# Kernel tuning notes

Hardware: AMD Instinct MI355X
Metric: run time of the kernel (lower is better)

Reference implementation:

```python
import jax, jax.numpy as jnp
import numpy as np

SHIFTS = [1, 3, 5, 7]
C = 16  # in_channels // 4
# -1 neighbor offsets for tmp1..tmp8 (dy, dx) in units of the dilation
OFFSETS = [(-1, -1), (-1, 0), (-1, 1), (0, 1), (1, 1), (1, 0), (1, -1), (0, -1)]


def setup_inputs() -> dict:
    key = jax.random.key(0)
    ks = jax.random.split(key, 32)
    d = {}
    d['cen'] = jax.random.normal(ks[0], (8, 64, 256, 256), jnp.float32)
    d['mas'] = jax.random.normal(ks[1], (8, 1, 256, 256), jnp.float32)
    d['in_conv_w'] = jax.random.normal(ks[2], (16, 64), jnp.float32) * 0.1
    d['in_conv_b'] = jax.random.normal(ks[3], (16,), jnp.float32) * 0.1
    for i, s in enumerate(SHIFTS):
        d[f'dw_w{s}'] = jax.random.normal(ks[4 + 2 * i], (16, 1, s, s), jnp.float32) * 0.1
        d[f'dw_b{s}'] = jax.random.normal(ks[5 + 2 * i], (16,), jnp.float32) * 0.1
    d['l1_w'] = jax.random.normal(ks[12], (4, 16, 4), jnp.float32) * 0.1
    d['l1_b'] = jax.random.normal(ks[13], (4, 16), jnp.float32) * 0.1
    d['l2_w'] = jax.random.normal(ks[14], (4, 16, 8), jnp.float32) * 0.1
    d['l2_b'] = jax.random.normal(ks[15], (4, 16), jnp.float32) * 0.1
    d['base_w'] = jax.random.normal(ks[16], (16, 4), jnp.float32) * 0.1
    d['bn_scale'] = jnp.ones((16,), jnp.float32)
    d['bn_bias'] = jnp.zeros((16,), jnp.float32)
    d['final_w'] = jax.random.normal(ks[17], (1, 16), jnp.float32) * 0.1
    d['final_b'] = jax.random.normal(ks[18], (1,), jnp.float32) * 0.1
    return d


def _dw_conv(x, w, b, pad):
    # depthwise conv, groups == channels
    y = jax.lax.conv_general_dilated(
        x, w, window_strides=(1, 1), padding=[(pad, pad), (pad, pad)],
        dimension_numbers=('NCHW', 'OIHW', 'NCHW'), feature_group_count=x.shape[1])
    return y + b[None, :, None, None]


def _shifted(x, dy, dx, d):
    # zero-padded shift: out(y,x) = in(y+dy, x+dx)
    H, W = x.shape[2], x.shape[3]
    p = jnp.pad(x, ((0, 0), (0, 0), (d, d), (d, d)))
    return p[:, :, d + dy:d + dy + H, d + dx:d + dx + W]


def _circ_shift(x, dw_w, dw_b, w1, b1, w2, b2, shift):
    x = _dw_conv(x, dw_w, dw_b, shift // 2)
    # tmp_k = x - x shifted by the k-th neighbor offset (dilation = shift)
    T = [x - _shifted(x, dy * shift, dx * shift, shift) for dy, dx in OFFSETS]
    # paired sums: S[k] = tmp_{k+1} + tmp_{k+5} (S repeats with period 4)
    S = [T[k] + T[k + 4] for k in range(4)]
    outs = []
    for k in range(8):  # fixed small structural loop
        feats = jnp.stack([S[(k + 1) % 4], S[(k + 3) % 4], S[(k + 2) % 4],
                           2.0 * T[(k + 4) % 8]], axis=2)  # (B,C,4,H,W)
        # grouped 1x1 conv (groups=C, 4C->C) == per-channel contraction over feature axis
        o = jnp.einsum('bcfhw,cf->bchw', feats, w1) + b1[None, :, None, None]
        outs.append(o * T[k])
    O = jnp.sort(jnp.stack(outs, axis=2), axis=2)  # (B,C,8,H,W) sorted over branch axis
    return jnp.einsum('bcfhw,cf->bchw', O, w2) + b2[None, :, None, None]


def reference(cen, mas, in_conv_w, in_conv_b, dw_w1, dw_b1, dw_w3, dw_b3,
              dw_w5, dw_b5, dw_w7, dw_b7, l1_w, l1_b, l2_w, l2_b,
              base_w, bn_scale, bn_bias, final_w, final_b):
    # in_conv: 1x1, in_channels -> C
    x = jnp.einsum('bihw,oi->bohw', cen, in_conv_w) + in_conv_b[None, :, None, None]
    dws = [(dw_w1, dw_b1), (dw_w3, dw_b3), (dw_w5, dw_b5), (dw_w7, dw_b7)]
    branches = [
        _circ_shift(x, dws[i][0], dws[i][1], l1_w[i], l1_b[i], l2_w[i], l2_b[i], SHIFTS[i])
        for i in range(len(SHIFTS))
    ]
    A = jnp.sort(jnp.stack(branches, axis=2), axis=2)  # (B,C,4,H,W)
    # out_conv: grouped 1x1 BaseConv (conv no-bias + BN(affine) + SiLU), then 1x1 -> 1, sigmoid
    y = jnp.einsum('bcfhw,cf->bchw', A, base_w)
    y = jax.nn.silu(y * bn_scale[None, :, None, None] + bn_bias[None, :, None, None])
    y = jnp.einsum('bchw,oc->bohw', y, final_w) + final_b[None, :, None, None]
    return jax.nn.sigmoid(y)
```

## Files before the change

kernel.cpp:

```cpp
#include <hip/hip_runtime.h>
#include <hip/hip_fp16.h>
#include <math.h>

#define HW 65536

typedef float v2f __attribute__((ext_vector_type(2), aligned(4)));
typedef _Float16 h2 __attribute__((ext_vector_type(2)));

__global__ __launch_bounds__(256) void k_inconv(const float* __restrict__ cen,
                                                const float* __restrict__ w,
                                                const float* __restrict__ bias,
                                                float* __restrict__ x) {
    __shared__ float sw[1024];
    __shared__ float sb[16];
    int tid = threadIdx.x;
    for (int i = tid; i < 1024; i += 256) sw[i] = w[i];
    if (tid < 16) sb[tid] = bias[tid];
    __syncthreads();

    long t  = (long)blockIdx.x * 256 + tid;
    long p0 = t * 2;
    int  b  = (int)(p0 >> 16);
    int  hw = (int)(p0 & 65535);

    const float2* src = (const float2*)(cen + ((long)b * 64) * HW + hw);
    float2 acc[16];
#pragma unroll
    for (int o = 0; o < 16; o++) { float bv = sb[o]; acc[o] = make_float2(bv, bv); }

#pragma unroll 8
    for (int i = 0; i < 64; i++) {
        float2 v = src[(long)i * (HW / 2)];
#pragma unroll
        for (int o = 0; o < 16; o++) {
            float wv = sw[o * 64 + i];
            acc[o].x = fmaf(v.x, wv, acc[o].x);
            acc[o].y = fmaf(v.y, wv, acc[o].y);
        }
    }
    float2* dst = (float2*)(x + ((long)b * 16) * HW + hw);
#pragma unroll
    for (int o = 0; o < 16; o++) dst[(long)o * (HW / 2)] = acc[o];
}

#define CEH(a, b) { h2 _t = __builtin_elementwise_min(a, b); \
                    b = __builtin_elementwise_max(a, b); a = _t; }

__device__ __forceinline__ void sort8_h2(h2* v) {
    CEH(v[0], v[1]); CEH(v[2], v[3]); CEH(v[4], v[5]); CEH(v[6], v[7]);
    CEH(v[0], v[2]); CEH(v[1], v[3]); CEH(v[4], v[6]); CEH(v[5], v[7]);
    CEH(v[1], v[2]); CEH(v[5], v[6]); CEH(v[0], v[4]); CEH(v[3], v[7]);
    CEH(v[1], v[5]); CEH(v[2], v[6]);
    CEH(v[1], v[4]); CEH(v[3], v[6]);
    CEH(v[2], v[4]); CEH(v[3], v[5]);
    CEH(v[3], v[4]);
}
__device__ __forceinline__ void sort4_h2(h2* v) {
    CEH(v[0], v[1]); CEH(v[2], v[3]); CEH(v[0], v[2]); CEH(v[1], v[3]); CEH(v[1], v[2]);
}

#define LXS 53
#define SS  47

__global__ __launch_bounds__(512, 4) void k_main(
    const float* __restrict__ x,
    const float* __restrict__ dw_w1, const float* __restrict__ dw_b1,
    const float* __restrict__ dw_w3, const float* __restrict__ dw_b3,
    const float* __restrict__ dw_w5, const float* __restrict__ dw_b5,
    const float* __restrict__ dw_w7, const float* __restrict__ dw_b7,
    const float* __restrict__ l1w, const float* __restrict__ l1b,
    const float* __restrict__ l2w, const float* __restrict__ l2b,
    const float* __restrict__ bw,  const float* __restrict__ bns,
    const float* __restrict__ bnb, __half* __restrict__ y16) {

    const int plane = blockIdx.y;
    const int c     = plane & 15;
    const int ty0   = (blockIdx.x >> 3) * 32;
    const int tx0   = (blockIdx.x & 7) * 32;
    const int tid   = threadIdx.x;

    __shared__ float lx[52 * LXS];
    __shared__ float lxs[4][46 * SS];

    const float* xp = x + (long)plane * HW;

    for (int i = tid; i < 52 * 52; i += 512) {
        int r  = i / 52;
        int cc = i - r * 52;
        int gy = ty0 - 10 + r, gx = tx0 - 10 + cc;
        float v = 0.f;
        if ((unsigned)gy < 256u && (unsigned)gx < 256u) v = xp[gy * 256 + gx];
        lx[r * LXS + cc] = v;
    }
    __syncthreads();

    const float* W7 = dw_w7 + c * 49;
    const float* W5 = dw_w5 + c * 25;
    const float* W3 = dw_w3 + c * 9;
    const float  W1 = dw_w1[c];
    const float  B1 = dw_b1[c], B3 = dw_b3[c], B5 = dw_b5[c], B7 = dw_b7[c];

    for (int u = tid; u < 46 * 23; u += 512) {
        int row = u / 23;
        int pc0 = (u - row * 23) * 2;
        float c7[2] = {0, 0}, c5[2] = {0, 0}, c3[2] = {0, 0}, c1[2] = {0, 0};
#pragma unroll
        for (int a = 0; a < 7; a++) {
            const float* rp = &lx[(row + a) * LXS + pc0];
            float v[9];
#pragma unroll
            for (int j = 0; j < 9; j++) v[j] = rp[j];
#pragma unroll
            for (int j = 0; j < 2; j++) {
#pragma unroll
                for (int bb = 0; bb < 7; bb++)
                    c7[j] = fmaf(v[j + bb], W7[a * 7 + bb], c7[j]);
                if (a >= 1 && a <= 5) {
#pragma unroll
                    for (int bb = 0; bb < 5; bb++)
                        c5[j] = fmaf(v[j + 1 + bb], W5[(a - 1) * 5 + bb], c5[j]);
                }
                if (a >= 2 && a <= 4) {
#pragma unroll
                    for (int bb = 0; bb < 3; bb++)
                        c3[j] = fmaf(v[j + 2 + bb], W3[(a - 2) * 3 + bb], c3[j]);
                }
                if (a == 3) c1[j] = v[j + 3] * W1;
            }
        }
        int gy  = ty0 - 7 + row;
        int gx0 = tx0 - 7 + pc0;
        bool rin = ((unsigned)gy < 256u);
        bool in0 = rin && ((unsigned)gx0 < 256u);
        bool in1 = rin && ((unsigned)(gx0 + 1) < 256u);
        int o = row * SS + pc0;
        lxs[0][o]     = in0 ? c1[0] + B1 : 0.f;
        lxs[0][o + 1] = in1 ? c1[1] + B1 : 0.f;
        lxs[1][o]     = in0 ? c3[0] + B3 : 0.f;
        lxs[1][o + 1] = in1 ? c3[1] + B3 : 0.f;
        lxs[2][o]     = in0 ? c5[0] + B5 : 0.f;
        lxs[2][o + 1] = in1 ? c5[1] + B5 : 0.f;
        lxs[3][o]     = in0 ? c7[0] + B7 : 0.f;
        lxs[3][o + 1] = in1 ? c7[1] + B7 : 0.f;
    }
    __syncthreads();

    const int ty  = tid >> 4;
    const int tx2 = (tid & 15) * 2;
    const int gy  = ty0 + ty, gx = tx0 + tx2;
    const int corner = ty * SS + tx2;

    h2 brh[4];
#pragma unroll
    for (int i = 0; i < 4; i++) {
        const int s = 1 + 2 * i;
        const float* xs = lxs[i];
        v2f ctr = *(const v2f*)&xs[corner + 7 * SS + 7];
        v2f n0  = *(const v2f*)&xs[corner + (7 - s) * SS + (7 - s)];
        v2f n1  = *(const v2f*)&xs[corner + (7 - s) * SS + 7];
        v2f n2  = *(const v2f*)&xs[corner + (7 - s) * SS + (7 + s)];
        v2f n3  = *(const v2f*)&xs[corner + 7 * SS + (7 + s)];
        v2f n4  = *(const v2f*)&xs[corner + (7 + s) * SS + (7 + s)];
        v2f n5  = *(const v2f*)&xs[corner + (7 + s) * SS + 7];
        v2f n6  = *(const v2f*)&xs[corner + (7 + s) * SS + (7 - s)];
        v2f n7  = *(const v2f*)&xs[corner + 7 * SS + (7 - s)];

        v2f T[8];
        T[0] = ctr - n0; T[1] = ctr - n1; T[2] = ctr - n2; T[3] = ctr - n3;
        T[4] = ctr - n4; T[5] = ctr - n5; T[6] = ctr - n6; T[7] = ctr - n7;
        v2f S[4];
#pragma unroll
        for (int k = 0; k < 4; k++) S[k] = T[k] + T[k + 4];

        const float w10   = l1w[i * 64 + c * 4 + 0];
        const float w11   = l1w[i * 64 + c * 4 + 1];
        const float w12   = l1w[i * 64 + c * 4 + 2];
        const float w13x2 = 2.f * l1w[i * 64 + c * 4 + 3];
        const float bb1   = l1b[i * 16 + c];

        v2f R[4];
#pragma unroll
        for (int m = 0; m < 4; m++) {
            v2f r = S[(m + 2) & 3] * w12 + bb1;
            r = S[(m + 3) & 3] * w11 + r;
            r = S[(m + 1) & 3] * w10 + r;
            R[m] = r;
        }

        h2 h8[8];
#pragma unroll
        for (int k = 0; k < 8; k++) {
            v2f o = (T[(k + 4) & 7] * w13x2 + R[k & 3]) * T[k];
            h8[k] = __builtin_convertvector(o, h2);
        }
        sort8_h2(h8);

        _Float16 l2bh = (_Float16)l2b[i * 16 + c];
        h2 acc = {l2bh, l2bh};
#pragma unroll
        for (int k = 0; k < 8; k++) {
            _Float16 wh = (_Float16)l2w[i * 128 + c * 8 + k];
            h2 wv = {wh, wh};
            acc = h8[k] * wv + acc;
        }
        brh[i] = acc;
    }

    sort4_h2(brh);
    h2 yvh = {(_Float16)0.f, (_Float16)0.f};
#pragma unroll
    for (int i = 0; i < 4; i++) {
        _Float16 bwh = (_Float16)bw[c * 4 + i];
        h2 bv = {bwh, bwh};
        yvh = brh[i] * bv + yvh;
    }
    const float bsc = bns[c], bbi = bnb[c];
    float zx = fmaf((float)yvh.x, bsc, bbi);
    float zy = fmaf((float)yvh.y, bsc, bbi);
    float sx = zx / (1.f + __expf(-zx));
    float sy = zy / (1.f + __expf(-zy));
    *(__half2*)&y16[(long)plane * HW + gy * 256 + gx] = __floats2half2_rn(sx, sy);
}

__global__ __launch_bounds__(256) void k_final(const __half* __restrict__ y16,
                                               const float* __restrict__ fw,
                                               const float* __restrict__ fb,
                                               float* __restrict__ out) {
    long t  = (long)blockIdx.x * 256 + threadIdx.x;
    long p0 = t * 2;
    int  b  = (int)(p0 >> 16);
    int  hw = (int)(p0 & 65535);

    float accx = fb[0], accy = fb[0];
#pragma unroll
    for (int cc = 0; cc < 16; cc++) {
        __half2 h = *(const __half2*)(y16 + (long)(b * 16 + cc) * HW + hw);
        float2 v = __half22float2(h);
        float wv = fw[cc];
        accx = fmaf(v.x, wv, accx);
        accy = fmaf(v.y, wv, accy);
    }
    float2 r;
    r.x = 1.f / (1.f + __expf(-accx));
    r.y = 1.f / (1.f + __expf(-accy));
    *(float2*)(out + p0) = r;
}

extern "C" void kernel_launch(void* const* d_in, const int* in_sizes, int n_in,
                              void* d_out, int out_size, void* d_ws, size_t ws_size,
                              hipStream_t stream) {
    (void)in_sizes; (void)n_in; (void)out_size; (void)ws_size;
    const float* cen   = (const float*)d_in[0];
    const float* in_w  = (const float*)d_in[2];
    const float* in_b  = (const float*)d_in[3];
    const float* dw_w1 = (const float*)d_in[4];
    const float* dw_b1 = (const float*)d_in[5];
    const float* dw_w3 = (const float*)d_in[6];
    const float* dw_b3 = (const float*)d_in[7];
    const float* dw_w5 = (const float*)d_in[8];
    const float* dw_b5 = (const float*)d_in[9];
    const float* dw_w7 = (const float*)d_in[10];
    const float* dw_b7 = (const float*)d_in[11];
    const float* l1w   = (const float*)d_in[12];
    const float* l1b   = (const float*)d_in[13];
    const float* l2w   = (const float*)d_in[14];
    const float* l2b   = (const float*)d_in[15];
    const float* bw    = (const float*)d_in[16];
    const float* bns   = (const float*)d_in[17];
    const float* bnb   = (const float*)d_in[18];
    const float* fw    = (const float*)d_in[19];
    const float* fb    = (const float*)d_in[20];

    float*  xbuf = (float*)d_ws;
    __half* y16  = (__half*)(xbuf + (size_t)8 * 16 * HW);
    float*  out  = (float*)d_out;

    k_inconv<<<1024, 256, 0, stream>>>(cen, in_w, in_b, xbuf);
    k_main<<<dim3(64, 128), 512, 0, stream>>>(xbuf, dw_w1, dw_b1, dw_w3, dw_b3,
                                              dw_w5, dw_b5, dw_w7, dw_b7,
                                              l1w, l1b, l2w, l2b, bw, bns, bnb, y16);
    k_final<<<1024, 256, 0, stream>>>(y16, fw, fb, out);
}
```

Baseline: 398.1 us.

## Split depthwise conv into separate kernel with fp16 intermediates and batch chunking

The fused main kernel, which recomputed depthwise convolutions over a 7-pixel halo per tile, is split into two kernels. k_dw computes the four depthwise outputs once per pixel and writes them as fp16 into padded global planes. k_px reloads those planes with halo to do the shift and sort stage. The in_conv output is now stored as fp16 and processes 4 pixels per thread. The two-kernel pair runs in 4 batch chunks of 2 images so the intermediate buffer can stay resident in cache. This removes redundant halo convolution work at the cost of extra global round trips, more kernel launches and fp16 precision loss on intermediates.

```diff
diff --git a/kernel.cpp b/kernel.cpp
--- a/kernel.cpp
+++ b/kernel.cpp
@@ -3,44 +3,142 @@
 #include <math.h>
 
 #define HW 65536
-
-typedef float v2f __attribute__((ext_vector_type(2), aligned(4)));
-typedef _Float16 h2 __attribute__((ext_vector_type(2)));
+#define XSTRIDE 272
+#define XPLANE (256 * XSTRIDE)
+
+typedef float    v2f __attribute__((ext_vector_type(2), aligned(4)));
+typedef float    f4  __attribute__((ext_vector_type(4)));
+typedef _Float16 h2  __attribute__((ext_vector_type(2)));
+typedef _Float16 h4  __attribute__((ext_vector_type(4)));
 
 __global__ __launch_bounds__(256) void k_inconv(const float* __restrict__ cen,
                                                 const float* __restrict__ w,
                                                 const float* __restrict__ bias,
-                                                float* __restrict__ x) {
-    __shared__ float sw[1024];
-    __shared__ float sb[16];
-    int tid = threadIdx.x;
-    for (int i = tid; i < 1024; i += 256) sw[i] = w[i];
-    if (tid < 16) sb[tid] = bias[tid];
-    __syncthreads();
-
-    long t  = (long)blockIdx.x * 256 + tid;
-    long p0 = t * 2;
+                                                __half* __restrict__ xh) {
+    long t  = (long)blockIdx.x * 256 + threadIdx.x;
+    long p0 = t * 4;
     int  b  = (int)(p0 >> 16);
     int  hw = (int)(p0 & 65535);
 
-    const float2* src = (const float2*)(cen + ((long)b * 64) * HW + hw);
-    float2 acc[16];
-#pragma unroll
-    for (int o = 0; o < 16; o++) { float bv = sb[o]; acc[o] = make_float2(bv, bv); }
-
-#pragma unroll 8
+    const float4* src = (const float4*)(cen + ((long)b * 64) * HW + hw);
+    float4 acc[16];
+#pragma unroll
+    for (int o = 0; o < 16; o++) { float bv = bias[o]; acc[o] = make_float4(bv, bv, bv, bv); }
+
+#pragma unroll 4
     for (int i = 0; i < 64; i++) {
-        float2 v = src[(long)i * (HW / 2)];
+        float4 v = src[(long)i * (HW / 4)];
 #pragma unroll
         for (int o = 0; o < 16; o++) {
-            float wv = sw[o * 64 + i];
+            float wv = w[o * 64 + i];
             acc[o].x = fmaf(v.x, wv, acc[o].x);
             acc[o].y = fmaf(v.y, wv, acc[o].y);
-        }
-    }
-    float2* dst = (float2*)(x + ((long)b * 16) * HW + hw);
-#pragma unroll
-    for (int o = 0; o < 16; o++) dst[(long)o * (HW / 2)] = acc[o];
+            acc[o].z = fmaf(v.z, wv, acc[o].z);
+            acc[o].w = fmaf(v.w, wv, acc[o].w);
+        }
+    }
+#pragma unroll
+    for (int o = 0; o < 16; o++) {
+        __half2 lo = __floats2half2_rn(acc[o].x, acc[o].y);
+        __half2 hi = __floats2half2_rn(acc[o].z, acc[o].w);
+        __half2* dst = (__half2*)(xh + ((long)(b * 16 + o)) * HW + hw);
+        dst[0] = lo;
+        dst[1] = hi;
+    }
+}
+
+__global__ __launch_bounds__(256) void k_dw(
+    const __half* __restrict__ xh,
+    const float* __restrict__ dw_w1, const float* __restrict__ dw_b1,
+    const float* __restrict__ dw_w3, const float* __restrict__ dw_b3,
+    const float* __restrict__ dw_w5, const float* __restrict__ dw_b5,
+    const float* __restrict__ dw_w7, const float* __restrict__ dw_b7,
+    _Float16* __restrict__ xs, int cb) {
+
+    const int pl  = blockIdx.y;
+    const int c   = pl & 15;
+    const int bl  = pl >> 4;
+    const int b   = cb * 2 + bl;
+    const int ty0 = (blockIdx.x >> 3) * 32;
+    const int tx0 = (blockIdx.x & 7) * 32;
+    const int tid = threadIdx.x;
+
+    __shared__ float lx[38 * 40];
+
+    const __half* xp = xh + (long)(b * 16 + c) * HW;
+    for (int i = tid; i < 38 * 38; i += 256) {
+        int r  = i / 38;
+        int cc = i - r * 38;
+        int gy = ty0 - 3 + r, gx = tx0 - 3 + cc;
+        float v = 0.f;
+        if ((unsigned)gy < 256u && (unsigned)gx < 256u) v = __half2float(xp[gy * 256 + gx]);
+        lx[r * 40 + cc] = v;
+    }
+    __syncthreads();
+
+    const float* W7 = dw_w7 + c * 49;
+    const float* W5 = dw_w5 + c * 25;
+    const float* W3 = dw_w3 + c * 9;
+    const float  W1 = dw_w1[c];
+    const float  B1 = dw_b1[c], B3 = dw_b3[c], B5 = dw_b5[c], B7 = dw_b7[c];
+
+    const int ty  = tid >> 3;
+    const int tx4 = (tid & 7) * 4;
+
+    float a7[4] = {0, 0, 0, 0}, a5[4] = {0, 0, 0, 0};
+    float a3[4] = {0, 0, 0, 0}, a1[4] = {0, 0, 0, 0};
+#pragma unroll
+    for (int a = 0; a < 7; a++) {
+        const float4* rp = (const float4*)&lx[(ty + a) * 40 + tx4];
+        float4 v0 = rp[0], v1 = rp[1], v2 = rp[2];
+        float v[12] = {v0.x, v0.y, v0.z, v0.w, v1.x, v1.y, v1.z, v1.w,
+                       v2.x, v2.y, v2.z, v2.w};
+#pragma unroll
+        for (int j = 0; j < 4; j++) {
+#pragma unroll
+            for (int bb = 0; bb < 7; bb++)
+                a7[j] = fmaf(v[j + bb], W7[a * 7 + bb], a7[j]);
+            if (a >= 1 && a <= 5) {
+#pragma unroll
+                for (int bb = 0; bb < 5; bb++)
+                    a5[j] = fmaf(v[j + 1 + bb], W5[(a - 1) * 5 + bb], a5[j]);
+            }
+            if (a >= 2 && a <= 4) {
+#pragma unroll
+                for (int bb = 0; bb < 3; bb++)
+                    a3[j] = fmaf(v[j + 2 + bb], W3[(a - 2) * 3 + bb], a3[j]);
+            }
+            if (a == 3) a1[j] = v[j + 3] * W1;
+        }
+    }
+
+    const long pb  = (long)pl * 4;
+    const long row = (long)(ty0 + ty) * XSTRIDE + 8 + tx0 + tx4;
+    f4 s;
+    s = (f4){a1[0] + B1, a1[1] + B1, a1[2] + B1, a1[3] + B1};
+    *(h4*)&xs[(pb + 0) * XPLANE + row] = __builtin_convertvector(s, h4);
+    s = (f4){a3[0] + B3, a3[1] + B3, a3[2] + B3, a3[3] + B3};
+    *(h4*)&xs[(pb + 1) * XPLANE + row] = __builtin_convertvector(s, h4);
+    s = (f4){a5[0] + B5, a5[1] + B5, a5[2] + B5, a5[3] + B5};
+    *(h4*)&xs[(pb + 2) * XPLANE + row] = __builtin_convertvector(s, h4);
+    s = (f4){a7[0] + B7, a7[1] + B7, a7[2] + B7, a7[3] + B7};
+    *(h4*)&xs[(pb + 3) * XPLANE + row] = __builtin_convertvector(s, h4);
+
+    h4 z = {(_Float16)0.f, (_Float16)0.f, (_Float16)0.f, (_Float16)0.f};
+    if (tx0 == 0 && tid < 64) {
+        int r  = tid >> 1;
+        int cc = (tid & 1) * 4;
+        long rr = (long)(ty0 + r) * XSTRIDE + cc;
+#pragma unroll
+        for (int i = 0; i < 4; i++) *(h4*)&xs[(pb + i) * XPLANE + rr] = z;
+    }
+    if (tx0 == 224 && tid < 64) {
+        int r  = tid >> 1;
+        int cc = 264 + (tid & 1) * 4;
+        long rr = (long)(ty0 + r) * XSTRIDE + cc;
+#pragma unroll
+        for (int i = 0; i < 4; i++) *(h4*)&xs[(pb + i) * XPLANE + rr] = z;
+    }
 }
 
 #define CEH(a, b) { h2 _t = __builtin_elementwise_min(a, b); \
@@ -59,111 +157,60 @@
     CEH(v[0], v[1]); CEH(v[2], v[3]); CEH(v[0], v[2]); CEH(v[1], v[3]); CEH(v[1], v[2]);
 }
 
-#define LXS 53
-#define SS  47
-
-__global__ __launch_bounds__(512, 4) void k_main(
-    const float* __restrict__ x,
-    const float* __restrict__ dw_w1, const float* __restrict__ dw_b1,
-    const float* __restrict__ dw_w3, const float* __restrict__ dw_b3,
-    const float* __restrict__ dw_w5, const float* __restrict__ dw_b5,
-    const float* __restrict__ dw_w7, const float* __restrict__ dw_b7,
+#define SS 48
+
+__global__ __launch_bounds__(512) void k_px(
+    const _Float16* __restrict__ xs,
     const float* __restrict__ l1w, const float* __restrict__ l1b,
     const float* __restrict__ l2w, const float* __restrict__ l2b,
     const float* __restrict__ bw,  const float* __restrict__ bns,
-    const float* __restrict__ bnb, __half* __restrict__ y16) {
-
-    const int plane = blockIdx.y;
-    const int c     = plane & 15;
-    const int ty0   = (blockIdx.x >> 3) * 32;
-    const int tx0   = (blockIdx.x & 7) * 32;
-    const int tid   = threadIdx.x;
-
-    __shared__ float lx[52 * LXS];
-    __shared__ float lxs[4][46 * SS];
-
-    const float* xp = x + (long)plane * HW;
-
-    for (int i = tid; i < 52 * 52; i += 512) {
-        int r  = i / 52;
-        int cc = i - r * 52;
-        int gy = ty0 - 10 + r, gx = tx0 - 10 + cc;
-        float v = 0.f;
-        if ((unsigned)gy < 256u && (unsigned)gx < 256u) v = xp[gy * 256 + gx];
-        lx[r * LXS + cc] = v;
-    }
-    __syncthreads();
-
-    const float* W7 = dw_w7 + c * 49;
-    const float* W5 = dw_w5 + c * 25;
-    const float* W3 = dw_w3 + c * 9;
-    const float  W1 = dw_w1[c];
-    const float  B1 = dw_b1[c], B3 = dw_b3[c], B5 = dw_b5[c], B7 = dw_b7[c];
-
-    for (int u = tid; u < 46 * 23; u += 512) {
-        int row = u / 23;
-        int pc0 = (u - row * 23) * 2;
-        float c7[2] = {0, 0}, c5[2] = {0, 0}, c3[2] = {0, 0}, c1[2] = {0, 0};
-#pragma unroll
-        for (int a = 0; a < 7; a++) {
-            const float* rp = &lx[(row + a) * LXS + pc0];
-            float v[9];
-#pragma unroll
-            for (int j = 0; j < 9; j++) v[j] = rp[j];
-#pragma unroll
-            for (int j = 0; j < 2; j++) {
-#pragma unroll
-                for (int bb = 0; bb < 7; bb++)
-                    c7[j] = fmaf(v[j + bb], W7[a * 7 + bb], c7[j]);
-                if (a >= 1 && a <= 5) {
-#pragma unroll
-                    for (int bb = 0; bb < 5; bb++)
-                        c5[j] = fmaf(v[j + 1 + bb], W5[(a - 1) * 5 + bb], c5[j]);
-                }
-                if (a >= 2 && a <= 4) {
-#pragma unroll
-                    for (int bb = 0; bb < 3; bb++)
-                        c3[j] = fmaf(v[j + 2 + bb], W3[(a - 2) * 3 + bb], c3[j]);
-                }
-                if (a == 3) c1[j] = v[j + 3] * W1;
-            }
-        }
-        int gy  = ty0 - 7 + row;
-        int gx0 = tx0 - 7 + pc0;
-        bool rin = ((unsigned)gy < 256u);
-        bool in0 = rin && ((unsigned)gx0 < 256u);
-        bool in1 = rin && ((unsigned)(gx0 + 1) < 256u);
-        int o = row * SS + pc0;
-        lxs[0][o]     = in0 ? c1[0] + B1 : 0.f;
-        lxs[0][o + 1] = in1 ? c1[1] + B1 : 0.f;
-        lxs[1][o]     = in0 ? c3[0] + B3 : 0.f;
-        lxs[1][o + 1] = in1 ? c3[1] + B3 : 0.f;
-        lxs[2][o]     = in0 ? c5[0] + B5 : 0.f;
-        lxs[2][o + 1] = in1 ? c5[1] + B5 : 0.f;
-        lxs[3][o]     = in0 ? c7[0] + B7 : 0.f;
-        lxs[3][o + 1] = in1 ? c7[1] + B7 : 0.f;
+    const float* __restrict__ bnb, __half* __restrict__ y16, int cb) {
+
+    const int pl  = blockIdx.y;
+    const int c   = pl & 15;
+    const int bl  = pl >> 4;
+    const int b   = cb * 2 + bl;
+    const int ty0 = (blockIdx.x >> 3) * 32;
+    const int tx0 = (blockIdx.x & 7) * 32;
+    const int tid = threadIdx.x;
+
+    __shared__ float sxs[4][46 * SS];
+
+    const _Float16* base = xs + (long)pl * 4 * XPLANE;
+    for (int idx = tid; idx < 4 * 46 * 12; idx += 512) {
+        int br  = idx / 552;
+        int rem = idx - br * 552;
+        int r   = rem / 12;
+        int seg = rem - r * 12;
+        int gy  = ty0 - 7 + r;
+        f4 val = {0.f, 0.f, 0.f, 0.f};
+        if ((unsigned)gy < 256u) {
+            h4 hv = *(const h4*)&base[(long)br * XPLANE + (long)gy * XSTRIDE + tx0 + seg * 4];
+            val = __builtin_convertvector(hv, f4);
+        }
+        *(f4*)&sxs[br][r * SS + seg * 4] = val;
     }
     __syncthreads();
 
     const int ty  = tid >> 4;
     const int tx2 = (tid & 15) * 2;
     const int gy  = ty0 + ty, gx = tx0 + tx2;
-    const int corner = ty * SS + tx2;
+    const int ci  = (ty + 7) * SS + tx2 + 8;
 
     h2 brh[4];
 #pragma unroll
     for (int i = 0; i < 4; i++) {
         const int s = 1 + 2 * i;
-        const float* xs = lxs[i];
-        v2f ctr = *(const v2f*)&xs[corner + 7 * SS + 7];
-        v2f n0  = *(const v2f*)&xs[corner + (7 - s) * SS + (7 - s)];
-        v2f n1  = *(const v2f*)&xs[corner + (7 - s) * SS + 7];
-        v2f n2  = *(const v2f*)&xs[corner + (7 - s) * SS + (7 + s)];
-        v2f n3  = *(const v2f*)&xs[corner + 7 * SS + (7 + s)];
-        v2f n4  = *(const v2f*)&xs[corner + (7 + s) * SS + (7 + s)];
-        v2f n5  = *(const v2f*)&xs[corner + (7 + s) * SS + 7];
-        v2f n6  = *(const v2f*)&xs[corner + (7 + s) * SS + (7 - s)];
-        v2f n7  = *(const v2f*)&xs[corner + 7 * SS + (7 - s)];
+        const float* xp = &sxs[i][ci];
+        v2f ctr = *(const v2f*)xp;
+        v2f n0  = *(const v2f*)(xp - s * SS - s);
+        v2f n1  = *(const v2f*)(xp - s * SS);
+        v2f n2  = *(const v2f*)(xp - s * SS + s);
+        v2f n3  = *(const v2f*)(xp + s);
+        v2f n4  = *(const v2f*)(xp + s * SS + s);
+        v2f n5  = *(const v2f*)(xp + s * SS);
+        v2f n6  = *(const v2f*)(xp + s * SS - s);
+        v2f n7  = *(const v2f*)(xp - s);
 
         v2f T[8];
         T[0] = ctr - n0; T[1] = ctr - n1; T[2] = ctr - n2; T[3] = ctr - n3;
@@ -219,7 +266,7 @@
     float zy = fmaf((float)yvh.y, bsc, bbi);
     float sx = zx / (1.f + __expf(-zx));
     float sy = zy / (1.f + __expf(-zy));
-    *(__half2*)&y16[(long)plane * HW + gy * 256 + gx] = __floats2half2_rn(sx, sy);
+    *(__half2*)&y16[(long)(b * 16 + c) * HW + gy * 256 + gx] = __floats2half2_rn(sx, sy);
 }
 
 __global__ __launch_bounds__(256) void k_final(const __half* __restrict__ y16,
@@ -271,13 +318,17 @@
     const float* fw    = (const float*)d_in[19];
     const float* fb    = (const float*)d_in[20];
 
-    float*  xbuf = (float*)d_ws;
-    __half* y16  = (__half*)(xbuf + (size_t)8 * 16 * HW);
-    float*  out  = (float*)d_out;
-
-    k_inconv<<<1024, 256, 0, stream>>>(cen, in_w, in_b, xbuf);
-    k_main<<<dim3(64, 128), 512, 0, stream>>>(xbuf, dw_w1, dw_b1, dw_w3, dw_b3,
-                                              dw_w5, dw_b5, dw_w7, dw_b7,
-                                              l1w, l1b, l2w, l2b, bw, bns, bnb, y16);
+    __half*   xh  = (__half*)d_ws;
+    _Float16* xs  = (_Float16*)(xh + (size_t)8 * 16 * HW);
+    __half*   y16 = (__half*)(xs + (size_t)128 * XPLANE);
+    float*    out = (float*)d_out;
+
+    k_inconv<<<512, 256, 0, stream>>>(cen, in_w, in_b, xh);
+    for (int cb = 0; cb < 4; cb++) {
+        k_dw<<<dim3(64, 32), 256, 0, stream>>>(xh, dw_w1, dw_b1, dw_w3, dw_b3,
+                                               dw_w5, dw_b5, dw_w7, dw_b7, xs, cb);
+        k_px<<<dim3(64, 32), 512, 0, stream>>>(xs, l1w, l1b, l2w, l2b, bw,
+                                               bns, bnb, y16, cb);
+    }
     k_final<<<1024, 256, 0, stream>>>(y16, fw, fb, out);
 }
```

Measured after the change: 397.0 us. No clear change (-0.3%).
